# Performance work log

Measured on AMD Instinct MI355X. Metric: run time of the kernel, lower is better.

Reference implementation:

```python
import jax, jax.numpy as jnp
import numpy as np

N_NODES, N_EDGES, N_GRAPHS, N_FEATS = 100000, 1600000, 256, 128
BN_EPS = 1e-5


def setup_inputs() -> dict:
    key = jax.random.key(0)
    ks = jax.random.split(key, 12)
    x = jax.random.normal(ks[0], (N_NODES, N_FEATS), jnp.float32)
    edge_index = jax.random.randint(ks[1], (2, N_EDGES), 0, N_NODES, dtype=jnp.int64)
    batch = jnp.sort(jax.random.randint(ks[2], (N_NODES,), 0, N_GRAPHS, dtype=jnp.int64))
    s = 0.05
    return {
        "x": x,
        "edge_index": edge_index,
        "batch": batch,
        "W1": jax.random.normal(ks[3], (N_FEATS, 32), jnp.float32) * s,
        "b1": jnp.zeros((32,), jnp.float32),
        "W2": jax.random.normal(ks[4], (32, 64), jnp.float32) * s,
        "b2": jnp.zeros((64,), jnp.float32),
        "fcW1": jax.random.normal(ks[5], (64, 32), jnp.float32) * s,
        "fcb1": jnp.zeros((32,), jnp.float32),
        "gamma": jnp.ones((32,), jnp.float32),
        "beta": jnp.zeros((32,), jnp.float32),
        "fcW2": jax.random.normal(ks[6], (32, 1), jnp.float32) * s,
        "fcb2": jnp.zeros((1,), jnp.float32),
    }


def _gcn_conv(x, src, dst, deg_inv, W, b):
    # PyG GCNConv: h = x @ W; out[d] = sum_e norm_e * h[src_e] + self-loop + b
    h = x @ W  # [N, out]
    norm = deg_inv[src] * deg_inv[dst]  # [E]
    msg = h[src] * norm[:, None]
    out = jax.ops.segment_sum(msg, dst, num_segments=x.shape[0])
    out = out + (deg_inv * deg_inv)[:, None] * h  # self-loop contribution
    return out + b


def reference(x, edge_index, batch, W1, b1, W2, b2, fcW1, fcb1, gamma, beta, fcW2, fcb2):
    src, dst = edge_index[0], edge_index[1]
    n = x.shape[0]
    # degree with self loops, computed on target nodes (PyG default)
    deg = 1.0 + jax.ops.segment_sum(jnp.ones_like(src, dtype=x.dtype), dst, num_segments=n)
    deg_inv = jax.lax.rsqrt(deg)
    h = _gcn_conv(x, src, dst, deg_inv, W1, b1)   # [N, 32]
    h = _gcn_conv(h, src, dst, deg_inv, W2, b2)   # [N, 64]
    # scatter_mean over graph batch
    sums = jax.ops.segment_sum(h, batch, num_segments=N_GRAPHS)  # [G, 64]
    cnt = jax.ops.segment_sum(jnp.ones((n,), h.dtype), batch, num_segments=N_GRAPHS)
    pooled = sums / jnp.maximum(cnt, 1.0)[:, None]
    # head: Linear -> ReLU -> BatchNorm1d (batch stats) -> Dropout(eval=id) -> Linear -> Softplus
    z = jax.nn.relu(pooled @ fcW1 + fcb1)  # [G, 32]
    mu = jnp.mean(z, axis=0)
    var = jnp.var(z, axis=0)
    z = (z - mu) * jax.lax.rsqrt(var + BN_EPS) * gamma + beta
    out = jax.nn.softplus(z @ fcW2 + fcb2)  # [G, 1]
    return out
```

## Files before the change

### kernel.cpp

```cpp
#include <hip/hip_runtime.h>

#define NN 100000
#define NE 1600000
#define NG 256

#define BSH 8
#define NPB 256
#define NBKT ((NN + NPB - 1) / NPB)
#define STRIDE 4608
#define TILE 8192
#define NB_P1 ((NE + TILE - 1) / TILE)

__device__ __forceinline__ unsigned short f2bf(float x) {
    unsigned int u = __float_as_uint(x);
    u += 0x7FFFu + ((u >> 16) & 1u);
    return (unsigned short)(u >> 16);
}
__device__ __forceinline__ float2 bf2x2(unsigned int v) {
    float2 r;
    r.x = __uint_as_float(v << 16);
    r.y = __uint_as_float(v & 0xFFFF0000u);
    return r;
}
__device__ __forceinline__ unsigned int bfpack(float x, float y) {
    return (unsigned int)f2bf(x) | ((unsigned int)f2bf(y) << 16);
}

__global__ __launch_bounds__(1024) void part_kernel(const int* __restrict__ src,
                                                    const int* __restrict__ dst,
                                                    int* __restrict__ bkt_cur,
                                                    int* __restrict__ epack) {
    __shared__ int hist[NBKT];
    __shared__ int cur[NBKT];
    int tid = threadIdx.x;
    int e0 = blockIdx.x * TILE;
    int e1 = min(e0 + TILE, NE);
    for (int i = tid; i < NBKT; i += 1024) hist[i] = 0;
    __syncthreads();
    for (int e = e0 + tid; e < e1; e += 1024)
        atomicAdd(&hist[dst[e] >> BSH], 1);
    __syncthreads();
    for (int i = tid; i < NBKT; i += 1024) {
        int h = hist[i];
        cur[i] = i * STRIDE + (h ? atomicAdd(&bkt_cur[i], h) : 0);
    }
    __syncthreads();
    for (int e = e0 + tid; e < e1; e += 1024) {
        int d = dst[e];
        int bk = d >> BSH;
        int pos = atomicAdd(&cur[bk], 1);
        if (pos < (bk + 1) * STRIDE)
            epack[pos] = src[e] | ((d & (NPB - 1)) << 17);
    }
}

__global__ __launch_bounds__(256) void build_kernel(const int* __restrict__ epack,
                                                    const int* __restrict__ bkt_cur,
                                                    int* __restrict__ row_beg,
                                                    int* __restrict__ row_deg,
                                                    int* __restrict__ col,
                                                    float* __restrict__ deg_inv) {
    __shared__ int cnt[NPB];
    __shared__ int ts[NPB];
    int b = blockIdx.x;
    int tid = threadIdx.x;
    int ebase = b * STRIDE;
    int eend = ebase + min(bkt_cur[b], STRIDE);
    int nbase = b << BSH;
    cnt[tid] = 0;
    __syncthreads();
    for (int e = ebase + tid; e < eend; e += 256)
        atomicAdd(&cnt[epack[e] >> 17], 1);
    __syncthreads();
    int v = cnt[tid];
    ts[tid] = v;
    __syncthreads();
    for (int off = 1; off < NPB; off <<= 1) {
        int t = (tid >= off) ? ts[tid - off] : 0;
        __syncthreads();
        ts[tid] += t;
        __syncthreads();
    }
    {
        int loff = ts[tid] - v;
        int node = nbase + tid;
        if (node < NN) {
            row_beg[node] = ebase + loff;
            row_deg[node] = v;
            deg_inv[node] = rsqrtf(1.0f + (float)v);
        }
        cnt[tid] = loff;
    }
    __syncthreads();
    for (int e = ebase + tid; e < eend; e += 256) {
        int rec = epack[e];
        int r = atomicAdd(&cnt[rec >> 17], 1);
        col[ebase + r] = rec & 0x1FFFF;
    }
}

__global__ __launch_bounds__(256) void gemm_x_w1(const float* __restrict__ x,
                                                 const float* __restrict__ W,
                                                 const float* __restrict__ deg_inv,
                                                 unsigned short* __restrict__ h, int N) {
    __shared__ float wsh[128 * 32];
    __shared__ float xs[32][132];
    int tid = threadIdx.x;
    int row0 = blockIdx.x * 32;
    for (int i = tid; i < 1024; i += 256)
        ((float4*)wsh)[i] = ((const float4*)W)[i];
    for (int i = tid; i < 1024; i += 256) {
        int r = i >> 5, c4 = i & 31;
        *(float4*)&xs[r][c4 * 4] = ((const float4*)(x + (size_t)(row0 + r) * 128))[c4];
    }
    __syncthreads();
    int r = tid >> 3;
    int c8 = (tid & 7) * 4;
    float acc0 = 0.f, acc1 = 0.f, acc2 = 0.f, acc3 = 0.f;
#pragma unroll
    for (int k0 = 0; k0 < 128; k0 += 4) {
        float4 xv = *(const float4*)&xs[r][k0];
#pragma unroll
        for (int j = 0; j < 4; ++j) {
            float xk = (&xv.x)[j];
            float4 wv = *(const float4*)&wsh[(k0 + j) * 32 + c8];
            acc0 += xk * wv.x;
            acc1 += xk * wv.y;
            acc2 += xk * wv.z;
            acc3 += xk * wv.w;
        }
    }
    float di = deg_inv[row0 + r];
    ushort4 o;
    o.x = f2bf(acc0 * di);
    o.y = f2bf(acc1 * di);
    o.z = f2bf(acc2 * di);
    o.w = f2bf(acc3 * di);
    *(ushort4*)&h[(size_t)(row0 + r) * 32 + c8] = o;
}

template <int MODE>
__global__ __launch_bounds__(256) void conv_bf_kernel(const int* __restrict__ row_beg,
                                                      const int* __restrict__ row_deg,
                                                      const int* __restrict__ col,
                                                      const uint2* __restrict__ h2,
                                                      const float* __restrict__ deg_inv,
                                                      const float* __restrict__ b,
                                                      uint2* __restrict__ out_bf,
                                                      float4* __restrict__ out_f32) {
    int gid = blockIdx.x * blockDim.x + threadIdx.x;
    int node = gid >> 3;
    int L = gid & 7;
    if (node >= NN) return;
    int beg = row_beg[node];
    int end = beg + row_deg[node];
    uint2 sv = h2[node * 8 + L];
    float2 s0 = bf2x2(sv.x), s1 = bf2x2(sv.y);
    float a00 = s0.x, a01 = s0.y, a02 = s1.x, a03 = s1.y;
    float a10 = 0.f, a11 = 0.f, a12 = 0.f, a13 = 0.f;
    float a20 = 0.f, a21 = 0.f, a22 = 0.f, a23 = 0.f;
    float a30 = 0.f, a31 = 0.f, a32 = 0.f, a33 = 0.f;
    for (int j0 = beg; j0 < end; j0 += 8) {
        int idx = j0 + L;
        int myc = (idx < end) ? col[idx] : 0;
        int m = end - j0;
        if (m > 8) m = 8;
        int t = 0;
        for (; t + 4 <= m; t += 4) {
            int c0 = __shfl(myc, t, 8);
            int c1 = __shfl(myc, t + 1, 8);
            int c2 = __shfl(myc, t + 2, 8);
            int c3 = __shfl(myc, t + 3, 8);
            uint2 v0 = h2[c0 * 8 + L];
            uint2 v1 = h2[c1 * 8 + L];
            uint2 v2 = h2[c2 * 8 + L];
            uint2 v3 = h2[c3 * 8 + L];
            float2 p0 = bf2x2(v0.x), q0 = bf2x2(v0.y);
            float2 p1 = bf2x2(v1.x), q1 = bf2x2(v1.y);
            float2 p2 = bf2x2(v2.x), q2 = bf2x2(v2.y);
            float2 p3 = bf2x2(v3.x), q3 = bf2x2(v3.y);
            a00 += p0.x; a01 += p0.y; a02 += q0.x; a03 += q0.y;
            a10 += p1.x; a11 += p1.y; a12 += q1.x; a13 += q1.y;
            a20 += p2.x; a21 += p2.y; a22 += q2.x; a23 += q2.y;
            a30 += p3.x; a31 += p3.y; a32 += q3.x; a33 += q3.y;
        }
        for (; t < m; ++t) {
            int c = __shfl(myc, t, 8);
            uint2 v = h2[c * 8 + L];
            float2 p = bf2x2(v.x), q = bf2x2(v.y);
            a00 += p.x; a01 += p.y; a02 += q.x; a03 += q.y;
        }
    }
    float c0 = (a00 + a10) + (a20 + a30);
    float c1 = (a01 + a11) + (a21 + a31);
    float c2 = (a02 + a12) + (a22 + a32);
    float c3 = (a03 + a13) + (a23 + a33);
    float di = deg_inv[node];
    if (MODE == 0) {
        float o0 = di * di * c0 + di * b[4 * L];
        float o1 = di * di * c1 + di * b[4 * L + 1];
        float o2 = di * di * c2 + di * b[4 * L + 2];
        float o3 = di * di * c3 + di * b[4 * L + 3];
        out_bf[node * 8 + L] = make_uint2(bfpack(o0, o1), bfpack(o2, o3));
    } else {
        out_f32[node * 8 + L] = make_float4(di * c0, di * c1, di * c2, di * c3);
    }
}

__global__ void pool_kernel(const float* __restrict__ h, const int* __restrict__ batch,
                            float* __restrict__ gsum, float* __restrict__ gcnt, int N) {
    int t = blockIdx.x * blockDim.x + threadIdx.x;
    int chunk = t / 32;
    int f = t % 32;
    int n0 = chunk * 16;
    if (n0 >= N) return;
    int n1 = min(n0 + 16, N);
    int cur = batch[n0];
    float acc = 0.f, ccnt = 0.f;
    for (int n = n0; n < n1; ++n) {
        int b = batch[n];
        if (b != cur) {
            unsafeAtomicAdd(&gsum[cur * 32 + f], acc);
            if (f == 0) unsafeAtomicAdd(&gcnt[cur], ccnt);
            acc = 0.f; ccnt = 0.f; cur = b;
        }
        acc += h[(size_t)n * 32 + f];
        ccnt += 1.f;
    }
    unsafeAtomicAdd(&gsum[cur * 32 + f], acc);
    if (f == 0) unsafeAtomicAdd(&gcnt[cur], ccnt);
}

__global__ __launch_bounds__(256) void head_kernel(const float* __restrict__ gsum,
                                                   const float* __restrict__ gcnt,
                                                   const float* __restrict__ W2,
                                                   const float* __restrict__ b2,
                                                   const float* __restrict__ fcW1,
                                                   const float* __restrict__ fcb1,
                                                   const float* __restrict__ gamma,
                                                   const float* __restrict__ beta,
                                                   const float* __restrict__ fcW2,
                                                   const float* __restrict__ fcb2,
                                                   float* __restrict__ out) {
    __shared__ float zs[NG][33];
    __shared__ float wcs[32 * 32];
    __shared__ float bcs[32];
    __shared__ float part1[8][32];
    __shared__ float part2[8][32];
    __shared__ float mu[32], rstd[32];
    int g = threadIdx.x;

    for (int idx = g; idx < 32 * 32; idx += 256) {
        int k = idx / 32, ch = idx % 32;
        float a = 0.f;
#pragma unroll
        for (int j = 0; j < 64; ++j) a += W2[k * 64 + j] * fcW1[j * 32 + ch];
        wcs[idx] = a;
    }
    if (g < 32) {
        float a = fcb1[g];
#pragma unroll
        for (int j = 0; j < 64; ++j) a += b2[j] * fcW1[j * 32 + g];
        bcs[g] = a;
    }
    __syncthreads();

    float p32[32];
    float inv = 1.0f / fmaxf(gcnt[g], 1.0f);
    {
        const float4* gs4 = (const float4*)(gsum + g * 32);
#pragma unroll
        for (int q = 0; q < 8; ++q) {
            float4 v = gs4[q];
            p32[q * 4 + 0] = v.x * inv;
            p32[q * 4 + 1] = v.y * inv;
            p32[q * 4 + 2] = v.z * inv;
            p32[q * 4 + 3] = v.w * inv;
        }
    }
#pragma unroll 4
    for (int ch = 0; ch < 32; ++ch) {
        float acc = bcs[ch];
#pragma unroll
        for (int k = 0; k < 32; ++k) acc += p32[k] * wcs[k * 32 + ch];
        zs[g][ch] = fmaxf(acc, 0.f);
    }
    __syncthreads();

    {
        int ch = g & 31, seg = g >> 5;
        float s = 0.f, sq = 0.f;
#pragma unroll
        for (int i = 0; i < 32; ++i) {
            float v = zs[seg * 32 + i][ch];
            s += v;
            sq += v * v;
        }
        part1[seg][ch] = s;
        part2[seg][ch] = sq;
    }
    __syncthreads();
    if (g < 32) {
        float s = 0.f, sq = 0.f;
#pragma unroll
        for (int i = 0; i < 8; ++i) { s += part1[i][g]; sq += part2[i][g]; }
        float m = s / NG;
        float v = sq / NG - m * m;
        mu[g] = m;
        rstd[g] = rsqrtf(fmaxf(v, 0.f) + 1e-5f);
    }
    __syncthreads();

    float acc = fcb2[0];
#pragma unroll 4
    for (int ch = 0; ch < 32; ++ch) {
        float zn = (zs[g][ch] - mu[ch]) * rstd[ch] * gamma[ch] + beta[ch];
        acc += zn * fcW2[ch];
    }
    out[g] = fmaxf(acc, 0.f) + log1pf(expf(-fabsf(acc)));
}

extern "C" void kernel_launch(void* const* d_in, const int* in_sizes, int n_in,
                              void* d_out, int out_size, void* d_ws, size_t ws_size,
                              hipStream_t stream) {
    const float* x     = (const float*)d_in[0];
    const int*   ei    = (const int*)d_in[1];
    const int*   batch = (const int*)d_in[2];
    const float* W1    = (const float*)d_in[3];
    const float* b1    = (const float*)d_in[4];
    const float* W2    = (const float*)d_in[5];
    const float* b2    = (const float*)d_in[6];
    const float* fcW1  = (const float*)d_in[7];
    const float* fcb1  = (const float*)d_in[8];
    const float* gamma = (const float*)d_in[9];
    const float* beta  = (const float*)d_in[10];
    const float* fcW2  = (const float*)d_in[11];
    const float* fcb2  = (const float*)d_in[12];
    float* out = (float*)d_out;

    char* p = (char*)d_ws;
    int*   bkt_cur = (int*)p;        p += 400 * 4;
    float* deg_inv = (float*)p;      p += (size_t)NN * 4;
    int*   row_beg = (int*)p;        p += (size_t)(NN + 8) * 4;
    int*   row_deg = (int*)p;        p += (size_t)(NN + 8) * 4;
    int*   epack   = (int*)p;        p += (size_t)NBKT * STRIDE * 4;
    int*   col     = (int*)p;        p += (size_t)NBKT * STRIDE * 4;
    unsigned short* h1s = (unsigned short*)p;  p += (size_t)NN * 32 * 2;
    uint2*          t1  = (uint2*)p;           p += (size_t)NN * 8 * 8;
    float* agg2    = (float*)p;      p += (size_t)NN * 32 * 4;
    float* gsum    = (float*)p;      p += (size_t)NG * 32 * 4;
    float* gcnt    = (float*)p;      p += (size_t)NG * 4;

    const int* srcv = ei;
    const int* dstv = ei + NE;

    hipMemsetAsync(bkt_cur, 0, NBKT * sizeof(int), stream);
    hipMemsetAsync(gsum, 0, (NG * 32 + NG) * sizeof(float), stream);

    part_kernel<<<NB_P1, 1024, 0, stream>>>(srcv, dstv, bkt_cur, epack);
    build_kernel<<<NBKT, 256, 0, stream>>>(epack, bkt_cur, row_beg, row_deg, col, deg_inv);

    gemm_x_w1<<<NN / 32, 256, 0, stream>>>(x, W1, deg_inv, h1s, NN);
    conv_bf_kernel<0><<<((size_t)NN * 8 + 255) / 256, 256, 0, stream>>>(
        row_beg, row_deg, col, (const uint2*)h1s, deg_inv, b1, t1, nullptr);

    conv_bf_kernel<1><<<((size_t)NN * 8 + 255) / 256, 256, 0, stream>>>(
        row_beg, row_deg, col, (const uint2*)t1, deg_inv, b1, nullptr, (float4*)agg2);

    pool_kernel<<<(((NN + 15) / 16) * 32 + 255) / 256, 256, 0, stream>>>(agg2, batch, gsum, gcnt, NN);
    head_kernel<<<1, 256, 0, stream>>>(gsum, gcnt, W2, b2, fcW1, fcb1, gamma, beta, fcW2, fcb2, out);
}
```

Before: 243.0 us.

## Stage edge partition in LDS, widen build blocks, fuse pooling into second conv

The partition kernel now keeps each tile's edges in registers, computes bucket offsets with a block prefix scan, stages the packed records in LDS sorted by bucket, and then writes them out contiguously. This aims for coalesced epack writes instead of scattered ones. The build kernel moves to 512 threads per block. The second conv kernel now does the graph mean-pool sums itself, reducing the two boundary graphs of each block in LDS, so the agg2 buffer and pool kernel are dropped and the two memsets are merged into one. The cost is larger LDS use in partition, which may lower occupancy, and global atomics for nodes outside those two graphs. Removing the early return in conv relies on NN being divisible by 32.

```diff
diff --git a/kernel.cpp b/kernel.cpp
--- a/kernel.cpp
+++ b/kernel.cpp
@@ -30,31 +30,70 @@
                                                     const int* __restrict__ dst,
                                                     int* __restrict__ bkt_cur,
                                                     int* __restrict__ epack) {
-    __shared__ int hist[NBKT];
+    __shared__ int hist[512];
+    __shared__ int scan0[512];
     __shared__ int cur[NBKT];
+    __shared__ int gbase[NBKT];
+    __shared__ int stage[TILE];
+    __shared__ unsigned short sb[TILE];
     int tid = threadIdx.x;
     int e0 = blockIdx.x * TILE;
     int e1 = min(e0 + TILE, NE);
-    for (int i = tid; i < NBKT; i += 1024) hist[i] = 0;
-    __syncthreads();
-    for (int e = e0 + tid; e < e1; e += 1024)
-        atomicAdd(&hist[dst[e] >> BSH], 1);
-    __syncthreads();
-    for (int i = tid; i < NBKT; i += 1024) {
-        int h = hist[i];
-        cur[i] = i * STRIDE + (h ? atomicAdd(&bkt_cur[i], h) : 0);
-    }
-    __syncthreads();
-    for (int e = e0 + tid; e < e1; e += 1024) {
-        int d = dst[e];
-        int bk = d >> BSH;
-        int pos = atomicAdd(&cur[bk], 1);
-        if (pos < (bk + 1) * STRIDE)
-            epack[pos] = src[e] | ((d & (NPB - 1)) << 17);
-    }
-}
-
-__global__ __launch_bounds__(256) void build_kernel(const int* __restrict__ epack,
+    int n = e1 - e0;
+
+    for (int i = tid; i < 512; i += 1024) hist[i] = 0;
+    __syncthreads();
+
+    int d_[8], s_[8];
+#pragma unroll
+    for (int k = 0; k < 8; ++k) {
+        int e = e0 + tid + k * 1024;
+        if (e < e1) {
+            d_[k] = dst[e];
+            s_[k] = src[e];
+            atomicAdd(&hist[d_[k] >> BSH], 1);
+        }
+    }
+    __syncthreads();
+
+    if (tid < 512) scan0[tid] = hist[tid];
+    __syncthreads();
+    for (int off = 1; off < 512; off <<= 1) {
+        int t = (tid < 512 && tid >= off) ? scan0[tid - off] : 0;
+        __syncthreads();
+        if (tid < 512) scan0[tid] += t;
+        __syncthreads();
+    }
+    if (tid < NBKT) {
+        int h = hist[tid];
+        int ex = scan0[tid] - h;
+        cur[tid] = ex;
+        gbase[tid] = tid * STRIDE + (h ? atomicAdd(&bkt_cur[tid], h) : 0) - ex;
+    }
+    __syncthreads();
+
+#pragma unroll
+    for (int k = 0; k < 8; ++k) {
+        int e = e0 + tid + k * 1024;
+        if (e < e1) {
+            int d = d_[k];
+            int bk = d >> BSH;
+            int p = atomicAdd(&cur[bk], 1);
+            stage[p] = s_[k] | ((d & (NPB - 1)) << 17);
+            sb[p] = (unsigned short)bk;
+        }
+    }
+    __syncthreads();
+
+    for (int j = tid; j < n; j += 1024) {
+        int bk = sb[j];
+        int a = gbase[bk] + j;
+        if (a < (bk + 1) * STRIDE)
+            epack[a] = stage[j];
+    }
+}
+
+__global__ __launch_bounds__(512) void build_kernel(const int* __restrict__ epack,
                                                     const int* __restrict__ bkt_cur,
                                                     int* __restrict__ row_beg,
                                                     int* __restrict__ row_deg,
@@ -67,21 +106,24 @@
     int ebase = b * STRIDE;
     int eend = ebase + min(bkt_cur[b], STRIDE);
     int nbase = b << BSH;
-    cnt[tid] = 0;
-    __syncthreads();
-    for (int e = ebase + tid; e < eend; e += 256)
+    if (tid < NPB) cnt[tid] = 0;
+    __syncthreads();
+    for (int e = ebase + tid; e < eend; e += 512)
         atomicAdd(&cnt[epack[e] >> 17], 1);
     __syncthreads();
-    int v = cnt[tid];
-    ts[tid] = v;
+    int v = 0;
+    if (tid < NPB) {
+        v = cnt[tid];
+        ts[tid] = v;
+    }
     __syncthreads();
     for (int off = 1; off < NPB; off <<= 1) {
-        int t = (tid >= off) ? ts[tid - off] : 0;
-        __syncthreads();
-        ts[tid] += t;
-        __syncthreads();
-    }
-    {
+        int t = (tid < NPB && tid >= off) ? ts[tid - off] : 0;
+        __syncthreads();
+        if (tid < NPB) ts[tid] += t;
+        __syncthreads();
+    }
+    if (tid < NPB) {
         int loff = ts[tid] - v;
         int node = nbase + tid;
         if (node < NN) {
@@ -92,7 +134,7 @@
         cnt[tid] = loff;
     }
     __syncthreads();
-    for (int e = ebase + tid; e < eend; e += 256) {
+    for (int e = ebase + tid; e < eend; e += 512) {
         int rec = epack[e];
         int r = atomicAdd(&cnt[rec >> 17], 1);
         col[ebase + r] = rec & 0x1FFFF;
@@ -147,11 +189,24 @@
                                                       const float* __restrict__ deg_inv,
                                                       const float* __restrict__ b,
                                                       uint2* __restrict__ out_bf,
-                                                      float4* __restrict__ out_f32) {
-    int gid = blockIdx.x * blockDim.x + threadIdx.x;
+                                                      const int* __restrict__ batch,
+                                                      float* __restrict__ gsum,
+                                                      float* __restrict__ gcnt) {
+    __shared__ float sacc[2][32];
+    __shared__ float scnt[2];
+    __shared__ int sg[2];
+    int tid = threadIdx.x;
+    int gid = blockIdx.x * 256 + tid;
     int node = gid >> 3;
     int L = gid & 7;
-    if (node >= NN) return;
+    if (MODE == 1) {
+        if (tid < 64) sacc[tid >> 5][tid & 31] = 0.f;
+        if (tid < 2) scnt[tid] = 0.f;
+        if (tid == 0) {
+            sg[0] = batch[(size_t)blockIdx.x * 32];
+            sg[1] = batch[(size_t)blockIdx.x * 32 + 31];
+        }
+    }
     int beg = row_beg[node];
     int end = beg + row_deg[node];
     uint2 sv = h2[node * 8 + L];
@@ -203,32 +258,38 @@
         float o3 = di * di * c3 + di * b[4 * L + 3];
         out_bf[node * 8 + L] = make_uint2(bfpack(o0, o1), bfpack(o2, o3));
     } else {
-        out_f32[node * 8 + L] = make_float4(di * c0, di * c1, di * c2, di * c3);
-    }
-}
-
-__global__ void pool_kernel(const float* __restrict__ h, const int* __restrict__ batch,
-                            float* __restrict__ gsum, float* __restrict__ gcnt, int N) {
-    int t = blockIdx.x * blockDim.x + threadIdx.x;
-    int chunk = t / 32;
-    int f = t % 32;
-    int n0 = chunk * 16;
-    if (n0 >= N) return;
-    int n1 = min(n0 + 16, N);
-    int cur = batch[n0];
-    float acc = 0.f, ccnt = 0.f;
-    for (int n = n0; n < n1; ++n) {
-        int b = batch[n];
-        if (b != cur) {
-            unsafeAtomicAdd(&gsum[cur * 32 + f], acc);
-            if (f == 0) unsafeAtomicAdd(&gcnt[cur], ccnt);
-            acc = 0.f; ccnt = 0.f; cur = b;
-        }
-        acc += h[(size_t)n * 32 + f];
-        ccnt += 1.f;
-    }
-    unsafeAtomicAdd(&gsum[cur * 32 + f], acc);
-    if (f == 0) unsafeAtomicAdd(&gcnt[cur], ccnt);
+        float o0 = di * c0, o1 = di * c1, o2 = di * c2, o3 = di * c3;
+        __syncthreads();
+        int gn = batch[node];
+        int base = 4 * L;
+        if (gn == sg[0]) {
+            atomicAdd(&sacc[0][base + 0], o0);
+            atomicAdd(&sacc[0][base + 1], o1);
+            atomicAdd(&sacc[0][base + 2], o2);
+            atomicAdd(&sacc[0][base + 3], o3);
+            if (L == 0) atomicAdd(&scnt[0], 1.f);
+        } else if (gn == sg[1]) {
+            atomicAdd(&sacc[1][base + 0], o0);
+            atomicAdd(&sacc[1][base + 1], o1);
+            atomicAdd(&sacc[1][base + 2], o2);
+            atomicAdd(&sacc[1][base + 3], o3);
+            if (L == 0) atomicAdd(&scnt[1], 1.f);
+        } else {
+            unsafeAtomicAdd(&gsum[gn * 32 + base + 0], o0);
+            unsafeAtomicAdd(&gsum[gn * 32 + base + 1], o1);
+            unsafeAtomicAdd(&gsum[gn * 32 + base + 2], o2);
+            unsafeAtomicAdd(&gsum[gn * 32 + base + 3], o3);
+            if (L == 0) unsafeAtomicAdd(&gcnt[gn], 1.f);
+        }
+        __syncthreads();
+        if (tid < 64) {
+            int s = tid >> 5, f = tid & 31;
+            if (s == 0 || sg[1] != sg[0])
+                unsafeAtomicAdd(&gsum[sg[s] * 32 + f], sacc[s][f]);
+        }
+        if (tid == 0) unsafeAtomicAdd(&gcnt[sg[0]], scnt[0]);
+        if (tid == 1 && sg[1] != sg[0]) unsafeAtomicAdd(&gcnt[sg[1]], scnt[1]);
+    }
 }
 
 __global__ __launch_bounds__(256) void head_kernel(const float* __restrict__ gsum,
@@ -340,6 +401,8 @@
 
     char* p = (char*)d_ws;
     int*   bkt_cur = (int*)p;        p += 400 * 4;
+    float* gsum    = (float*)p;      p += (size_t)NG * 32 * 4;
+    float* gcnt    = (float*)p;      p += (size_t)NG * 4;
     float* deg_inv = (float*)p;      p += (size_t)NN * 4;
     int*   row_beg = (int*)p;        p += (size_t)(NN + 8) * 4;
     int*   row_deg = (int*)p;        p += (size_t)(NN + 8) * 4;
@@ -347,26 +410,21 @@
     int*   col     = (int*)p;        p += (size_t)NBKT * STRIDE * 4;
     unsigned short* h1s = (unsigned short*)p;  p += (size_t)NN * 32 * 2;
     uint2*          t1  = (uint2*)p;           p += (size_t)NN * 8 * 8;
-    float* agg2    = (float*)p;      p += (size_t)NN * 32 * 4;
-    float* gsum    = (float*)p;      p += (size_t)NG * 32 * 4;
-    float* gcnt    = (float*)p;      p += (size_t)NG * 4;
 
     const int* srcv = ei;
     const int* dstv = ei + NE;
 
-    hipMemsetAsync(bkt_cur, 0, NBKT * sizeof(int), stream);
-    hipMemsetAsync(gsum, 0, (NG * 32 + NG) * sizeof(float), stream);
+    hipMemsetAsync(bkt_cur, 0, 400 * 4 + (size_t)NG * 32 * 4 + (size_t)NG * 4, stream);
 
     part_kernel<<<NB_P1, 1024, 0, stream>>>(srcv, dstv, bkt_cur, epack);
-    build_kernel<<<NBKT, 256, 0, stream>>>(epack, bkt_cur, row_beg, row_deg, col, deg_inv);
+    build_kernel<<<NBKT, 512, 0, stream>>>(epack, bkt_cur, row_beg, row_deg, col, deg_inv);
 
     gemm_x_w1<<<NN / 32, 256, 0, stream>>>(x, W1, deg_inv, h1s, NN);
     conv_bf_kernel<0><<<((size_t)NN * 8 + 255) / 256, 256, 0, stream>>>(
-        row_beg, row_deg, col, (const uint2*)h1s, deg_inv, b1, t1, nullptr);
+        row_beg, row_deg, col, (const uint2*)h1s, deg_inv, b1, t1, nullptr, nullptr, nullptr);
 
     conv_bf_kernel<1><<<((size_t)NN * 8 + 255) / 256, 256, 0, stream>>>(
-        row_beg, row_deg, col, (const uint2*)t1, deg_inv, b1, nullptr, (float4*)agg2);
-
-    pool_kernel<<<(((NN + 15) / 16) * 32 + 255) / 256, 256, 0, stream>>>(agg2, batch, gsum, gcnt, NN);
+        row_beg, row_deg, col, (const uint2*)t1, deg_inv, b1, nullptr, batch, gsum, gcnt);
+
     head_kernel<<<1, 256, 0, stream>>>(gsum, gcnt, W2, b2, fcW1, fcb1, gamma, beta, fcW2, fcb2, out);
 }
```

After: 227.1 us. -6.5%, faster.
